# Kernel tuning notes

Measured on AMD Instinct MI355X. Metric: run time of the kernel, lower is better.

Reference implementation:

```python
import jax, jax.numpy as jnp
import numpy as np

B, T, C = 2, 2048, 2048
H = 16
ROPE_DIM, NOPE_DIM, V_DIM = 64, 64, 128
HEAD_DIM = NOPE_DIM + ROPE_DIM  # 128
Q_RANK, KV_RANK = 1536, 512


def setup_inputs() -> dict:
    key = jax.random.key(0)
    ks = jax.random.split(key, 8)
    std = 0.02
    return {
        "x": jax.random.normal(ks[0], (B, T, C), jnp.float32),
        "cos": jax.random.normal(ks[1], (1, T, 1, ROPE_DIM // 2), jnp.float32),
        "sin": jax.random.normal(ks[2], (1, T, 1, ROPE_DIM // 2), jnp.float32),
        "wq_down": jax.random.normal(ks[3], (Q_RANK, C), jnp.float32) * std,
        "wq_up": jax.random.normal(ks[4], (H * HEAD_DIM, Q_RANK), jnp.float32) * std,
        "wkv_down": jax.random.normal(ks[5], (KV_RANK, C), jnp.float32) * std,
        "wkv_up": jax.random.normal(ks[6], (H * (HEAD_DIM + V_DIM), KV_RANK), jnp.float32) * std,
        "wo": jax.random.normal(ks[7], (C, H * V_DIM), jnp.float32) * std,
    }


def _rope(x, cos, sin):
    # x: [B, T, H, rope_dim]
    d = x.shape[-1] // 2
    x1, x2 = x[..., :d], x[..., d:]
    return jnp.concatenate([x1 * cos + x2 * sin, -x1 * sin + x2 * cos], axis=-1)


def _rms_norm(x):
    eps = jnp.finfo(x.dtype).eps
    return x * jax.lax.rsqrt(jnp.mean(jnp.square(x), axis=-1, keepdims=True) + eps)


def reference(x, cos, sin, wq_down, wq_up, wkv_down, wkv_up, wo):
    # Low-rank q projection
    q = jnp.einsum('btc,rc,dr->btd', x, wq_down, wq_up)
    q = q.reshape(B, T, H, HEAD_DIM)
    q_nope, q_rope = q[..., :NOPE_DIM], q[..., NOPE_DIM:]
    # Low-rank kv projection (naive decompression)
    kv = jnp.einsum('btc,rc,dr->btd', x, wkv_down, wkv_up)
    kv = kv.reshape(B, T, H, HEAD_DIM + V_DIM)
    k_nope = kv[..., :NOPE_DIM]
    k_rope = kv[..., NOPE_DIM:HEAD_DIM]
    v = kv[..., HEAD_DIM:]
    # Partial RoPE on the rope sub-dims only
    q_rope = _rope(q_rope, cos, sin)
    k_rope = _rope(k_rope, cos, sin)
    q = _rms_norm(jnp.concatenate([q_nope, q_rope], axis=-1))
    k = _rms_norm(jnp.concatenate([k_nope, k_rope], axis=-1))
    # Causal SDPA: [B, H, T, T]
    scale = 1.0 / jnp.sqrt(jnp.float32(HEAD_DIM))
    scores = jnp.einsum('bthd,bshd->bhts', q, k) * scale
    causal = jnp.tril(jnp.ones((T, T), dtype=bool))
    scores = jnp.where(causal, scores, jnp.finfo(scores.dtype).min)
    probs = jax.nn.softmax(scores, axis=-1)
    y = jnp.einsum('bhts,bshd->bthd', probs, v).reshape(B, T, H * V_DIM)
    return y @ wo.T
```

## Files before the change

kernel.cpp:

```cpp
#include <hip/hip_runtime.h>
#include <hip/hip_bf16.h>
#include <math.h>
#include <type_traits>

#define AS1 __attribute__((address_space(1)))
#define AS3 __attribute__((address_space(3)))

typedef __bf16  bf16x8 __attribute__((ext_vector_type(8)));
typedef float   f32x4  __attribute__((ext_vector_type(4)));
typedef __hip_bfloat16 bf16;

#define MFMA16x16x32 __builtin_amdgcn_mfma_f32_16x16x32_bf16

__device__ __forceinline__ void gload16(const void* g, void* l) {
  __builtin_amdgcn_global_load_lds((const AS1 void*)g, (AS3 void*)l, 16, 0, 0);
}

__device__ __forceinline__ unsigned short bfbits(float v) {
  return __builtin_bit_cast(unsigned short, __float2bfloat16(v));
}

struct CastArgs {
  const float4* src[6];
  ushort4* dst[6];
  unsigned bound[6];
};

__global__ __launch_bounds__(256) void f2bf_multi(CastArgs a) {
  unsigned i = blockIdx.x * 256 + threadIdx.x;
  if (i >= a.bound[5]) return;
  unsigned lo = 0;
  int s = 0;
#pragma unroll
  for (int k = 0; k < 5; k++) {
    if (i >= a.bound[k]) { s = k + 1; lo = a.bound[k]; }
  }
  unsigned idx = i - lo;
  float4 v = a.src[s][idx];
  ushort4 o;
  o.x = bfbits(v.x); o.y = bfbits(v.y); o.z = bfbits(v.z); o.w = bfbits(v.w);
  a.dst[s][idx] = o;
}

template <typename OutT>
__global__ __launch_bounds__(256, 3) void gemm_bt(const bf16* __restrict__ A,
                                                  const bf16* __restrict__ W,
                                                  OutT* __restrict__ Cp,
                                                  int M, int N, int K, int lda) {
  __shared__ __align__(16) bf16 As[128 * 32];
  __shared__ __align__(16) bf16 Ws[128 * 32];
  const int t = threadIdx.x;
  const int w = t >> 6, lane = t & 63;
  const int quad = lane >> 4, l16 = lane & 15;
  const int wr = (w >> 1) * 64, wc = (w & 1) * 64;
  const size_t m0 = (size_t)blockIdx.x * 128;
  const size_t n0 = (size_t)blockIdx.y * 128;
  const int rowS = t >> 2;
  const int kch  = (t & 3) * 8;

  f32x4 acc[4][4];
#pragma unroll
  for (int i = 0; i < 4; i++)
#pragma unroll
    for (int j = 0; j < 4; j++) acc[i][j] = f32x4{0.f, 0.f, 0.f, 0.f};

  for (int k0 = 0; k0 < K; k0 += 32) {
    __syncthreads();
    gload16(A + (m0 + rowS) * (size_t)lda + k0 + kch,      (char*)As + w * 1024);
    gload16(A + (m0 + rowS + 64) * (size_t)lda + k0 + kch, (char*)As + 4096 + w * 1024);
    gload16(W + (n0 + rowS) * (size_t)K + k0 + kch,        (char*)Ws + w * 1024);
    gload16(W + (n0 + rowS + 64) * (size_t)K + k0 + kch,   (char*)Ws + 4096 + w * 1024);
    __syncthreads();

    bf16x8 af[4], bw[4];
#pragma unroll
    for (int i = 0; i < 4; i++)
      af[i] = *(const bf16x8*)(As + (wr + i * 16 + l16) * 32 + quad * 8);
#pragma unroll
    for (int j = 0; j < 4; j++)
      bw[j] = *(const bf16x8*)(Ws + (wc + j * 16 + l16) * 32 + quad * 8);
#pragma unroll
    for (int i = 0; i < 4; i++)
#pragma unroll
      for (int j = 0; j < 4; j++)
        acc[i][j] = MFMA16x16x32(af[i], bw[j], acc[i][j], 0, 0, 0);
  }

#pragma unroll
  for (int i = 0; i < 4; i++)
#pragma unroll
    for (int j = 0; j < 4; j++)
#pragma unroll
      for (int r = 0; r < 4; r++) {
        size_t row = m0 + wr + i * 16 + quad * 4 + r;
        size_t col = n0 + wc + j * 16 + l16;
        float v = acc[i][j][r];
        if constexpr (std::is_same<OutT, float>::value)
          Cp[row * N + col] = v;
        else
          Cp[row * N + col] = __float2bfloat16(v);
      }
}

__global__ __launch_bounds__(256, 3) void gemm_kvup(const bf16* __restrict__ A,
                                                    const bf16* __restrict__ W,
                                                    bf16* __restrict__ kvraw,
                                                    bf16* __restrict__ vT) {
  __shared__ __align__(16) bf16 As[128 * 32];
  __shared__ __align__(16) bf16 Ws[128 * 32];
  const int t = threadIdx.x;
  const int w = t >> 6, lane = t & 63;
  const int quad = lane >> 4, l16 = lane & 15;
  const int wr = (w >> 1) * 64, wc = (w & 1) * 64;
  const size_t m0 = (size_t)blockIdx.x * 128;
  const int n0 = (int)blockIdx.y * 128;
  const int rowS = t >> 2;
  const int kch  = (t & 3) * 8;
  const int K = 512, lda = 2048;

  f32x4 acc[4][4];
#pragma unroll
  for (int i = 0; i < 4; i++)
#pragma unroll
    for (int j = 0; j < 4; j++) acc[i][j] = f32x4{0.f, 0.f, 0.f, 0.f};

  for (int k0 = 0; k0 < K; k0 += 32) {
    __syncthreads();
    gload16(A + (m0 + rowS) * (size_t)lda + k0 + kch,        (char*)As + w * 1024);
    gload16(A + (m0 + rowS + 64) * (size_t)lda + k0 + kch,   (char*)As + 4096 + w * 1024);
    gload16(W + ((size_t)n0 + rowS) * K + k0 + kch,          (char*)Ws + w * 1024);
    gload16(W + ((size_t)n0 + rowS + 64) * K + k0 + kch,     (char*)Ws + 4096 + w * 1024);
    __syncthreads();

    bf16x8 af[4], bw[4];
#pragma unroll
    for (int i = 0; i < 4; i++)
      af[i] = *(const bf16x8*)(As + (wr + i * 16 + l16) * 32 + quad * 8);
#pragma unroll
    for (int j = 0; j < 4; j++)
      bw[j] = *(const bf16x8*)(Ws + (wc + j * 16 + l16) * 32 + quad * 8);
#pragma unroll
    for (int i = 0; i < 4; i++)
#pragma unroll
      for (int j = 0; j < 4; j++)
        acc[i][j] = MFMA16x16x32(af[i], bw[j], acc[i][j], 0, 0, 0);
  }

  if ((n0 & 128) == 0) {
#pragma unroll
    for (int i = 0; i < 4; i++)
#pragma unroll
      for (int j = 0; j < 4; j++)
#pragma unroll
        for (int r = 0; r < 4; r++) {
          size_t row = m0 + wr + i * 16 + quad * 4 + r;
          size_t col = (size_t)n0 + wc + j * 16 + l16;
          kvraw[row * 4096 + col] = __float2bfloat16(acc[i][j][r]);
        }
  } else {
    const int h = n0 >> 8;
#pragma unroll
    for (int i = 0; i < 4; i++) {
      size_t row = m0 + wr + i * 16 + quad * 4;
      int bb = (int)(row >> 11), tloc = (int)(row & 2047);
#pragma unroll
      for (int j = 0; j < 4; j++) {
        int d = wc + j * 16 + l16;
        ushort4 v4;
        v4.x = bfbits(acc[i][j][0]);
        v4.y = bfbits(acc[i][j][1]);
        v4.z = bfbits(acc[i][j][2]);
        v4.w = bfbits(acc[i][j][3]);
        *(ushort4*)(vT + ((size_t)(bb * 16 + h) * 128 + d) * 2048 + tloc) = v4;
      }
    }
  }
}

__global__ __launch_bounds__(256) void rope_rms(const bf16* __restrict__ qraw,
                                                const bf16* __restrict__ kvraw,
                                                const float* __restrict__ cosp,
                                                const float* __restrict__ sinp,
                                                bf16* __restrict__ qn,
                                                bf16* __restrict__ kn) {
  const int bt = blockIdx.x;
  const int w = threadIdx.x >> 6, lane = threadIdx.x & 63;
  const int h = blockIdx.y * 4 + w;
  const int tt = bt & 2047;
  const float c = cosp[tt * 32 + (lane & 31)];
  const float s = sinp[tt * 32 + (lane & 31)];
  const float inv128 = 1.0f / 128.0f;
  const float eps = 1.1920929e-7f;

  {
    const bf16* base = qraw + (size_t)bt * 2048 + h * 128;
    float a = (float)base[lane];
    float o = (float)base[64 + lane];
    float partner = __shfl_xor(o, 32);
    float orope = (lane < 32) ? (o * c + partner * s) : (o * c - partner * s);
    float ss = a * a + orope * orope;
#pragma unroll
    for (int off = 1; off < 64; off <<= 1) ss += __shfl_xor(ss, off);
    float rn = rsqrtf(ss * inv128 + eps);
    bf16* outp = qn + ((size_t)bt * 16 + h) * 128;
    outp[lane] = __float2bfloat16(a * rn);
    outp[64 + lane] = __float2bfloat16(orope * rn);
  }
  {
    const bf16* base = kvraw + (size_t)bt * 4096 + h * 256;
    float a = (float)base[lane];
    float o = (float)base[64 + lane];
    float partner = __shfl_xor(o, 32);
    float orope = (lane < 32) ? (o * c + partner * s) : (o * c - partner * s);
    float ss = a * a + orope * orope;
#pragma unroll
    for (int off = 1; off < 64; off <<= 1) ss += __shfl_xor(ss, off);
    float rn = rsqrtf(ss * inv128 + eps);
    bf16* outp = kn + ((size_t)bt * 16 + h) * 128;
    outp[lane] = __float2bfloat16(a * rn);
    outp[64 + lane] = __float2bfloat16(orope * rn);
  }
}

__global__ __launch_bounds__(256, 4) void attn_kernel(const bf16* __restrict__ qn,
                                                      const bf16* __restrict__ kn,
                                                      const bf16* __restrict__ vT,
                                                      bf16* __restrict__ y) {
  __shared__ __align__(16) bf16 Ks[64 * 128];
  __shared__ __align__(16) bf16 Vs[128 * 64];
  __shared__ __align__(16) bf16 Ps[4][16 * 64];
  const int t = threadIdx.x, w = t >> 6, lane = t & 63;
  const int quad = lane >> 4, l16 = lane & 15;
  const int b = blockIdx.x >> 4, h = blockIdx.x & 15;
  const int yy = (int)blockIdx.y;
  const int y0 = yy & 7, k4 = yy >> 3;
  int xb;
  if (k4 == 0) xb = 31 - y0;
  else if (k4 == 1) xb = y0;
  else if (k4 == 2) xb = 23 - y0;
  else xb = 8 + y0;
  const int q0 = xb * 64;
  const int T_ = 2048, H_ = 16;

  bf16x8 qf[4];
  {
    const bf16* qbase = qn + ((size_t)(b * T_ + q0 + w * 16 + l16) * H_ + h) * 128;
#pragma unroll
    for (int ks = 0; ks < 4; ks++) qf[ks] = *(const bf16x8*)(qbase + ks * 32 + quad * 8);
  }
  f32x4 yacc[8];
#pragma unroll
  for (int i = 0; i < 8; i++) yacc[i] = f32x4{0.f, 0.f, 0.f, 0.f};
  float lrow[4] = {0.f, 0.f, 0.f, 0.f};
  const float K1 = 0.08838834764831845f * 1.4426950408889634f;
  const float K2 = -12.0f * 1.4426950408889634f;
  const int ntiles = xb + 1;

  for (int it = 0; it < ntiles; ++it) {
    const int s0 = it * 64;
    __syncthreads();
#pragma unroll
    for (int is = 0; is < 4; ++is) {
      int srow = is * 16 + w * 4 + quad;
      int cg = l16 ^ (srow & 7);
      gload16(kn + ((size_t)(b * T_ + s0 + srow) * H_ + h) * 128 + cg * 8,
              (char*)Ks + is * 4096 + w * 1024);
    }
#pragma unroll
    for (int is = 0; is < 4; ++is) {
      int drow = is * 32 + w * 8 + (lane >> 3);
      int cg = (lane & 7) ^ (drow & 7);
      gload16(vT + ((size_t)(b * H_ + h) * 128 + drow) * T_ + s0 + cg * 8,
              (char*)Vs + is * 4096 + w * 1024);
    }
    __syncthreads();

    f32x4 sacc[4];
#pragma unroll
    for (int cg = 0; cg < 4; cg++) sacc[cg] = f32x4{0.f, 0.f, 0.f, 0.f};
#pragma unroll
    for (int cg = 0; cg < 4; ++cg) {
      const int srow = cg * 16 + l16;
#pragma unroll
      for (int ks = 0; ks < 4; ++ks) {
        int pos = (ks * 4 + quad) ^ (srow & 7);
        bf16x8 kf = *(const bf16x8*)(Ks + srow * 128 + pos * 8);
        sacc[cg] = MFMA16x16x32(qf[ks], kf, sacc[cg], 0, 0, 0);
      }
    }

    const bool diag = (it == xb);
    float p[4][4];
#pragma unroll
    for (int cg = 0; cg < 4; ++cg)
#pragma unroll
      for (int r = 0; r < 4; ++r) {
        float e;
        if (diag && (cg * 16 + l16 > w * 16 + quad * 4 + r))
          e = 0.0f;
        else
          e = exp2f(fmaf(sacc[cg][r], K1, K2));
        p[cg][r] = e;
        lrow[r] += e;
      }

#pragma unroll
    for (int cg = 0; cg < 4; cg++)
#pragma unroll
      for (int r = 0; r < 4; r++) {
        const int row = quad * 4 + r;
        const int col = cg * 16 + l16;
        Ps[w][row * 64 + (((col >> 3) ^ (row & 7)) << 3) + (col & 7)] =
            __float2bfloat16(p[cg][r]);
      }
    __asm__ volatile("s_waitcnt lgkmcnt(0)" ::: "memory");

    bf16x8 pf[2];
#pragma unroll
    for (int k2 = 0; k2 < 2; k2++)
      pf[k2] = *(const bf16x8*)(&Ps[w][l16 * 64 + (((k2 * 4 + quad) ^ (l16 & 7)) << 3)]);
#pragma unroll
    for (int dg = 0; dg < 8; dg++) {
      const int drow = dg * 16 + l16;
#pragma unroll
      for (int k2 = 0; k2 < 2; k2++) {
        int pos = (k2 * 4 + quad) ^ (drow & 7);
        bf16x8 vf = *(const bf16x8*)(Vs + drow * 64 + pos * 8);
        yacc[dg] = MFMA16x16x32(pf[k2], vf, yacc[dg], 0, 0, 0);
      }
    }
  }

#pragma unroll
  for (int off = 1; off < 16; off <<= 1)
#pragma unroll
    for (int r = 0; r < 4; r++) lrow[r] += __shfl_xor(lrow[r], off);
#pragma unroll
  for (int r = 0; r < 4; r++) {
    float inv = 1.0f / lrow[r];
    size_t qrow = (size_t)(b * T_ + q0 + w * 16 + quad * 4 + r);
    bf16* outp = y + qrow * 2048 + h * 128;
#pragma unroll
    for (int dg = 0; dg < 8; dg++)
      outp[dg * 16 + l16] = __float2bfloat16(yacc[dg][r] * inv);
  }
}

extern "C" void kernel_launch(void* const* d_in, const int* in_sizes, int n_in,
                              void* d_out, int out_size, void* d_ws, size_t ws_size,
                              hipStream_t stream) {
  (void)in_sizes; (void)n_in; (void)out_size; (void)ws_size;
  const float* x    = (const float*)d_in[0];
  const float* cosp = (const float*)d_in[1];
  const float* sinp = (const float*)d_in[2];
  const float* wqd  = (const float*)d_in[3];
  const float* wqu  = (const float*)d_in[4];
  const float* wkvd = (const float*)d_in[5];
  const float* wkvu = (const float*)d_in[6];
  const float* wo   = (const float*)d_in[7];
  float* out = (float*)d_out;

  char* ws = (char*)d_ws;
  size_t off = 0;
  auto alloc = [&](size_t elems) { bf16* p = (bf16*)(ws + off); off += elems * 2; return p; };
  bf16* xb      = alloc((size_t)4096 * 2048);
  bf16* wqdB    = alloc((size_t)1536 * 2048);
  bf16* wkvdB   = alloc((size_t)512 * 2048);
  bf16* wquB    = alloc((size_t)2048 * 1536);
  bf16* wkvuB   = alloc((size_t)4096 * 512);
  bf16* woB     = alloc((size_t)2048 * 2048);
  bf16* qkvdown = alloc((size_t)4096 * 2048);
  bf16* qraw    = alloc((size_t)4096 * 2048);
  bf16* kvraw   = alloc((size_t)4096 * 4096);
  bf16* qnb     = alloc((size_t)4096 * 16 * 128);
  bf16* knb     = alloc((size_t)4096 * 16 * 128);
  bf16* vTb     = alloc((size_t)2 * 16 * 128 * 2048);
  bf16* yb      = alloc((size_t)4096 * 2048);

  CastArgs ca;
  const float* srcs[6] = {x, wqd, wkvd, wqu, wkvu, wo};
  bf16* dsts[6]        = {xb, wqdB, wkvdB, wquB, wkvuB, woB};
  size_t cnts[6] = {(size_t)4096 * 2048, (size_t)1536 * 2048, (size_t)512 * 2048,
                    (size_t)2048 * 1536, (size_t)4096 * 512,  (size_t)2048 * 2048};
  unsigned cum = 0;
  for (int i = 0; i < 6; i++) {
    ca.src[i] = (const float4*)srcs[i];
    ca.dst[i] = (ushort4*)dsts[i];
    cum += (unsigned)(cnts[i] / 4);
    ca.bound[i] = cum;
  }
  f2bf_multi<<<dim3((cum + 255) / 256), 256, 0, stream>>>(ca);

  gemm_bt<bf16><<<dim3(32, 16), 256, 0, stream>>>(xb, wqdB, qkvdown, 4096, 2048, 2048, 2048);
  gemm_bt<bf16><<<dim3(32, 16), 256, 0, stream>>>(qkvdown, wquB, qraw, 4096, 2048, 1536, 2048);
  gemm_kvup<<<dim3(32, 32), 256, 0, stream>>>(qkvdown + 1536, wkvuB, kvraw, vTb);
  rope_rms<<<dim3(4096, 4), 256, 0, stream>>>(qraw, kvraw, cosp, sinp, qnb, knb);
  attn_kernel<<<dim3(32, 32), 256, 0, stream>>>(qnb, knb, vTb, yb);
  gemm_bt<float><<<dim3(32, 16), 256, 0, stream>>>(yb, woB, out, 4096, 2048, 2048, 2048);
}
```

Baseline: 375.3 us.

## Double-buffer K/V tiles and pair causal query blocks per attention workgroup

The attention kernel now keeps two LDS buffers for K and V. It issues the global-to-LDS loads for the next tile before computing on the current one and waits with vmcnt, so memory latency overlaps with MFMA work. Each workgroup also processes two query blocks (31-pr and pr), which balances causal work evenly, and the grid y dimension is halved to 16. The cost is double the LDS use and launch_bounds lowered to 2 waves per SIMD, which cuts occupancy. There are also fewer workgroups, each running longer and serially.

```diff
diff --git a/kernel.cpp b/kernel.cpp
--- a/kernel.cpp
+++ b/kernel.cpp
@@ -222,127 +222,142 @@
   }
 }
 
-__global__ __launch_bounds__(256, 4) void attn_kernel(const bf16* __restrict__ qn,
+__global__ __launch_bounds__(256, 2) void attn_kernel(const bf16* __restrict__ qn,
                                                       const bf16* __restrict__ kn,
                                                       const bf16* __restrict__ vT,
                                                       bf16* __restrict__ y) {
-  __shared__ __align__(16) bf16 Ks[64 * 128];
-  __shared__ __align__(16) bf16 Vs[128 * 64];
+  __shared__ __align__(16) bf16 Ks[2][64 * 128];
+  __shared__ __align__(16) bf16 Vs[2][128 * 64];
   __shared__ __align__(16) bf16 Ps[4][16 * 64];
   const int t = threadIdx.x, w = t >> 6, lane = t & 63;
   const int quad = lane >> 4, l16 = lane & 15;
   const int b = blockIdx.x >> 4, h = blockIdx.x & 15;
-  const int yy = (int)blockIdx.y;
-  const int y0 = yy & 7, k4 = yy >> 3;
-  int xb;
-  if (k4 == 0) xb = 31 - y0;
-  else if (k4 == 1) xb = y0;
-  else if (k4 == 2) xb = 23 - y0;
-  else xb = 8 + y0;
-  const int q0 = xb * 64;
+  const int pr = (int)blockIdx.y;
   const int T_ = 2048, H_ = 16;
-
-  bf16x8 qf[4];
-  {
-    const bf16* qbase = qn + ((size_t)(b * T_ + q0 + w * 16 + l16) * H_ + h) * 128;
-#pragma unroll
-    for (int ks = 0; ks < 4; ks++) qf[ks] = *(const bf16x8*)(qbase + ks * 32 + quad * 8);
-  }
-  f32x4 yacc[8];
-#pragma unroll
-  for (int i = 0; i < 8; i++) yacc[i] = f32x4{0.f, 0.f, 0.f, 0.f};
-  float lrow[4] = {0.f, 0.f, 0.f, 0.f};
   const float K1 = 0.08838834764831845f * 1.4426950408889634f;
   const float K2 = -12.0f * 1.4426950408889634f;
-  const int ntiles = xb + 1;
-
-  for (int it = 0; it < ntiles; ++it) {
-    const int s0 = it * 64;
-    __syncthreads();
+
+  auto stage_tile = [&](int bufi, int it2) {
+    const int s0 = it2 * 64;
 #pragma unroll
     for (int is = 0; is < 4; ++is) {
       int srow = is * 16 + w * 4 + quad;
       int cg = l16 ^ (srow & 7);
       gload16(kn + ((size_t)(b * T_ + s0 + srow) * H_ + h) * 128 + cg * 8,
-              (char*)Ks + is * 4096 + w * 1024);
+              (char*)(&Ks[bufi][0]) + is * 4096 + w * 1024);
     }
 #pragma unroll
     for (int is = 0; is < 4; ++is) {
       int drow = is * 32 + w * 8 + (lane >> 3);
       int cg = (lane & 7) ^ (drow & 7);
       gload16(vT + ((size_t)(b * H_ + h) * 128 + drow) * T_ + s0 + cg * 8,
-              (char*)Vs + is * 4096 + w * 1024);
-    }
-    __syncthreads();
-
-    f32x4 sacc[4];
-#pragma unroll
-    for (int cg = 0; cg < 4; cg++) sacc[cg] = f32x4{0.f, 0.f, 0.f, 0.f};
-#pragma unroll
-    for (int cg = 0; cg < 4; ++cg) {
-      const int srow = cg * 16 + l16;
-#pragma unroll
-      for (int ks = 0; ks < 4; ++ks) {
-        int pos = (ks * 4 + quad) ^ (srow & 7);
-        bf16x8 kf = *(const bf16x8*)(Ks + srow * 128 + pos * 8);
-        sacc[cg] = MFMA16x16x32(qf[ks], kf, sacc[cg], 0, 0, 0);
+              (char*)(&Vs[bufi][0]) + is * 4096 + w * 1024);
+    }
+  };
+
+  for (int sidx = 0; sidx < 2; ++sidx) {
+    const int xb = sidx ? pr : (31 - pr);
+    const int q0 = xb * 64;
+    const int nt = xb + 1;
+
+    bf16x8 qf[4];
+    {
+      const bf16* qbase = qn + ((size_t)(b * T_ + q0 + w * 16 + l16) * H_ + h) * 128;
+#pragma unroll
+      for (int ks = 0; ks < 4; ks++) qf[ks] = *(const bf16x8*)(qbase + ks * 32 + quad * 8);
+    }
+    f32x4 yacc[8];
+#pragma unroll
+    for (int i = 0; i < 8; i++) yacc[i] = f32x4{0.f, 0.f, 0.f, 0.f};
+    float lrow[4] = {0.f, 0.f, 0.f, 0.f};
+
+    stage_tile(0, 0);
+    int cur = 0;
+
+    for (int it = 0; it < nt; ++it) {
+      if (it + 1 < nt) {
+        stage_tile(cur ^ 1, it + 1);
+        __asm__ volatile("s_waitcnt vmcnt(8)" ::: "memory");
+      } else {
+        __asm__ volatile("s_waitcnt vmcnt(0)" ::: "memory");
       }
-    }
-
-    const bool diag = (it == xb);
-    float p[4][4];
-#pragma unroll
-    for (int cg = 0; cg < 4; ++cg)
-#pragma unroll
-      for (int r = 0; r < 4; ++r) {
-        float e;
-        if (diag && (cg * 16 + l16 > w * 16 + quad * 4 + r))
-          e = 0.0f;
-        else
-          e = exp2f(fmaf(sacc[cg][r], K1, K2));
-        p[cg][r] = e;
-        lrow[r] += e;
+      __asm__ volatile("s_barrier" ::: "memory");
+
+      const bf16* Kc = &Ks[cur][0];
+      const bf16* Vc = &Vs[cur][0];
+
+      f32x4 sacc[4];
+#pragma unroll
+      for (int cg = 0; cg < 4; cg++) sacc[cg] = f32x4{0.f, 0.f, 0.f, 0.f};
+#pragma unroll
+      for (int cg = 0; cg < 4; ++cg) {
+        const int srow = cg * 16 + l16;
+#pragma unroll
+        for (int ks = 0; ks < 4; ++ks) {
+          int pos = (ks * 4 + quad) ^ (srow & 7);
+          bf16x8 kf = *(const bf16x8*)(Kc + srow * 128 + pos * 8);
+          sacc[cg] = MFMA16x16x32(qf[ks], kf, sacc[cg], 0, 0, 0);
+        }
       }
 
-#pragma unroll
-    for (int cg = 0; cg < 4; cg++)
-#pragma unroll
-      for (int r = 0; r < 4; r++) {
-        const int row = quad * 4 + r;
-        const int col = cg * 16 + l16;
-        Ps[w][row * 64 + (((col >> 3) ^ (row & 7)) << 3) + (col & 7)] =
-            __float2bfloat16(p[cg][r]);
+      const bool diag = (it == xb);
+      float p[4][4];
+#pragma unroll
+      for (int cg = 0; cg < 4; ++cg)
+#pragma unroll
+        for (int r = 0; r < 4; ++r) {
+          float e;
+          if (diag && (cg * 16 + l16 > w * 16 + quad * 4 + r))
+            e = 0.0f;
+          else
+            e = exp2f(fmaf(sacc[cg][r], K1, K2));
+          p[cg][r] = e;
+          lrow[r] += e;
+        }
+
+#pragma unroll
+      for (int cg = 0; cg < 4; cg++)
+#pragma unroll
+        for (int r = 0; r < 4; r++) {
+          const int row = quad * 4 + r;
+          const int col = cg * 16 + l16;
+          Ps[w][row * 64 + (((col >> 3) ^ (row & 7)) << 3) + (col & 7)] =
+              __float2bfloat16(p[cg][r]);
+        }
+      __asm__ volatile("s_waitcnt lgkmcnt(0)" ::: "memory");
+
+      bf16x8 pf[2];
+#pragma unroll
+      for (int k2 = 0; k2 < 2; k2++)
+        pf[k2] = *(const bf16x8*)(&Ps[w][l16 * 64 + (((k2 * 4 + quad) ^ (l16 & 7)) << 3)]);
+#pragma unroll
+      for (int dg = 0; dg < 8; dg++) {
+        const int drow = dg * 16 + l16;
+#pragma unroll
+        for (int k2 = 0; k2 < 2; k2++) {
+          int pos = (k2 * 4 + quad) ^ (drow & 7);
+          bf16x8 vf = *(const bf16x8*)(Vc + drow * 64 + pos * 8);
+          yacc[dg] = MFMA16x16x32(pf[k2], vf, yacc[dg], 0, 0, 0);
+        }
       }
-    __asm__ volatile("s_waitcnt lgkmcnt(0)" ::: "memory");
-
-    bf16x8 pf[2];
-#pragma unroll
-    for (int k2 = 0; k2 < 2; k2++)
-      pf[k2] = *(const bf16x8*)(&Ps[w][l16 * 64 + (((k2 * 4 + quad) ^ (l16 & 7)) << 3)]);
-#pragma unroll
-    for (int dg = 0; dg < 8; dg++) {
-      const int drow = dg * 16 + l16;
-#pragma unroll
-      for (int k2 = 0; k2 < 2; k2++) {
-        int pos = (k2 * 4 + quad) ^ (drow & 7);
-        bf16x8 vf = *(const bf16x8*)(Vs + drow * 64 + pos * 8);
-        yacc[dg] = MFMA16x16x32(pf[k2], vf, yacc[dg], 0, 0, 0);
-      }
-    }
-  }
-
-#pragma unroll
-  for (int off = 1; off < 16; off <<= 1)
-#pragma unroll
-    for (int r = 0; r < 4; r++) lrow[r] += __shfl_xor(lrow[r], off);
-#pragma unroll
-  for (int r = 0; r < 4; r++) {
-    float inv = 1.0f / lrow[r];
-    size_t qrow = (size_t)(b * T_ + q0 + w * 16 + quad * 4 + r);
-    bf16* outp = y + qrow * 2048 + h * 128;
-#pragma unroll
-    for (int dg = 0; dg < 8; dg++)
-      outp[dg * 16 + l16] = __float2bfloat16(yacc[dg][r] * inv);
+
+      __asm__ volatile("s_barrier" ::: "memory");
+      cur ^= 1;
+    }
+
+#pragma unroll
+    for (int off = 1; off < 16; off <<= 1)
+#pragma unroll
+      for (int r = 0; r < 4; r++) lrow[r] += __shfl_xor(lrow[r], off);
+#pragma unroll
+    for (int r = 0; r < 4; r++) {
+      float inv = 1.0f / lrow[r];
+      size_t qrow = (size_t)(b * T_ + q0 + w * 16 + quad * 4 + r);
+      bf16* outp = y + qrow * 2048 + h * 128;
+#pragma unroll
+      for (int dg = 0; dg < 8; dg++)
+        outp[dg * 16 + l16] = __float2bfloat16(yacc[dg][r] * inv);
+    }
   }
 }
 
@@ -395,6 +410,6 @@
   gemm_bt<bf16><<<dim3(32, 16), 256, 0, stream>>>(qkvdown, wquB, qraw, 4096, 2048, 1536, 2048);
   gemm_kvup<<<dim3(32, 32), 256, 0, stream>>>(qkvdown + 1536, wkvuB, kvraw, vTb);
   rope_rms<<<dim3(4096, 4), 256, 0, stream>>>(qraw, kvraw, cosp, sinp, qnb, knb);
-  attn_kernel<<<dim3(32, 32), 256, 0, stream>>>(qnb, knb, vTb, yb);
+  attn_kernel<<<dim3(32, 16), 256, 0, stream>>>(qnb, knb, vTb, yb);
   gemm_bt<float><<<dim3(32, 16), 256, 0, stream>>>(yb, woB, out, 4096, 2048, 2048, 2048);
 }
```

Result: no change. 371.7 us (-1.0%).
